# Optimization experiments

Measured on AMD Instinct MI355X. Metric: run time of the kernel, lower is better.

## Reference

```python
import jax, jax.numpy as jnp
import numpy as np

P = 16        # patch size
SIM = 0.3     # similarity threshold (forward default arg `sim`)
STY_STD = 1000.0


def patchify(imgs):
    # (N,3,H,W) -> (N, h*w, p*p*3)
    N, C, H, W = imgs.shape
    h, w = H // P, W // P
    x = imgs.reshape(N, C, h, P, w, P)
    x = jnp.einsum('nchpwq->nhwpqc', x)
    return x.reshape(N, h * w, P * P * C)


def setup_inputs() -> dict:
    key = jax.random.key(0)
    k1, k2, k3, k4 = jax.random.split(key, 4)
    N, L, D = 2, 196, 768
    x = jax.random.normal(k1, (N, L + 1, D), dtype=jnp.float32)
    imgs = jax.random.normal(k2, (N, 3, 224, 224), dtype=jnp.float32)
    # torch trunc_normal_(std=1000, a=-2, b=2) == truncated normal on [-2,2]
    learnable_sty = (jax.random.truncated_normal(
        k3, -2.0 / STY_STD, 2.0 / STY_STD, (N, L, L, 1), dtype=jnp.float32) * STY_STD)
    noise = jax.random.normal(k4, (N, L, L, 1), dtype=jnp.float32)
    return {"x": x, "imgs": imgs, "learnable_sty": learnable_sty, "noise": noise}


def reference(x, imgs, learnable_sty, noise):
    imgs = patchify(imgs)                                   # (N, L, 768)
    cls_tokens, x = x[:, :1], x[:, 1:]
    N, L, D = x.shape

    # per-patch normalization (torch.var default is unbiased -> ddof=1)
    mean = imgs.mean(axis=-1, keepdims=True)
    var = jnp.var(imgs, axis=-1, keepdims=True, ddof=1)
    imgs_n = (imgs - mean) / jnp.sqrt(var + 1e-6)
    nrm = jnp.linalg.norm(imgs_n, axis=-1)                  # (N, L)
    Sim = jnp.einsum('aik,ajk->aij', imgs_n, imgs_n) / (nrm[:, :, None] * nrm[:, None, :])

    M0 = jnp.triu((Sim > SIM).astype(jnp.float32))          # (N, L, L), binary
    rows = jnp.arange(L)

    def body(i, M):
        # original loop breaks when sum == N*L; we freeze M once that holds
        done = M.sum() == N * L
        mask = (M[:, i, :] == 0).astype(M.dtype)            # (N, L)
        # rows <= i unchanged (M*M == M for binary), rows > i masked
        upd = jnp.where(rows[None, :, None] > i, M * mask[:, None, :], M)
        return jnp.where(done, M, upd)

    M = jax.lax.fori_loop(0, L - 1, body, M0)

    # decompose: phase (con) keeps grad, amplitude (sty) is detached
    fft = jnp.fft.fftn(x, axes=(-1,))
    con, sty = jnp.angle(fft), jnp.abs(fft)
    sty_d = jax.lax.stop_gradient(sty)

    avg_sum = (M[..., None] * sty_d[:, None, :, :]).sum(axis=2)   # (N, L, D)
    sty_mask = (avg_sum > 0).astype(jnp.float32)                   # (N, L, D)
    num = M.sum(axis=2)[..., None]                                 # (N, L, 1)
    avg = avg_sum / jnp.clip(num, 1e-7, None)                      # (N, L, D)
    std = jnp.sqrt(
        (M[..., None] * (sty_d[:, None, :, :] - avg[:, :, None, :]) ** 2).sum(axis=2)
        / jnp.clip(num, 1e-7, None))                               # (N, L, D)

    sty_para = sty_mask[:, None, :, :] * learnable_sty             # (N, L, L, D)
    sty_para = sty_para / jnp.clip(sty_para.sum(axis=2, keepdims=True), 1e-7, None)
    various = noise * std[:, None, :, :] + avg[:, None, :, :]      # (N, L, L, D)
    sum_sty = (sty_para * various).sum(axis=2)                     # (N, L, D)

    # compose: ifft(amp * e^{i phase}), torch .float() keeps the real part
    out = jnp.real(jnp.fft.ifftn(sum_sty * jnp.exp(1j * con), axes=(-1,))).astype(jnp.float32)
    return jnp.concatenate((cls_tokens, out), axis=1)
```

## Files before the change

### kernel.cpp

```cpp
#include <hip/hip_runtime.h>
#include <math.h>

typedef unsigned long long u64;

#define NBATCH 2
#define LTOK 196
#define DDIM 768
#define NLD (NBATCH*LTOK*DDIM)

#ifndef M_PI
#define M_PI 3.14159265358979323846
#endif

#define S3 0.86602540378443864676f

__global__ __launch_bounds__(256) void k_patch(const float* __restrict__ imgs,
                                               float* __restrict__ u) {
  int blk = blockIdx.x;
  int a = blk / LTOK, l = blk - a * LTOK;
  int hh = l / 14, ww = l - hh * 14;
  int t = threadIdx.x;
  float loc[3];
  double s = 0.0, sq = 0.0;
#pragma unroll
  for (int e = 0; e < 3; e++) {
    int d = t + (e << 8);
    int p = d / 48, r = d - p * 48;
    int q2 = r / 3, c = r - q2 * 3;
    float val = imgs[((size_t)(a * 3 + c) * 224 + (hh * 16 + p)) * 224 + (ww * 16 + q2)];
    loc[e] = val;
    s += (double)val;
    sq += (double)val * (double)val;
  }
#pragma unroll
  for (int o = 32; o > 0; o >>= 1) { s += __shfl_down(s, o); sq += __shfl_down(sq, o); }
  __shared__ double rs[4], rq[4];
  __shared__ float sh_mu, sh_sc;
  if ((t & 63) == 0) { rs[t >> 6] = s; rq[t >> 6] = sq; }
  __syncthreads();
  if (t == 0) {
    double S = rs[0] + rs[1] + rs[2] + rs[3];
    double Q = rq[0] + rq[1] + rq[2] + rq[3];
    double mean = S / 768.0;
    double ss = Q - S * S / 768.0;
    if (ss < 1e-30) ss = 1e-30;
    sh_mu = (float)mean;
    sh_sc = (float)(1.0 / sqrt(ss));
  }
  __syncthreads();
  float mu = sh_mu, sc = sh_sc;
  size_t base = ((size_t)a * LTOK + l) * DDIM;
#pragma unroll
  for (int e = 0; e < 3; e++) { int d = t + (e << 8); u[base + d] = (loc[e] - mu) * sc; }
}

__device__ __forceinline__ void fft_butterfly(float* re, float* im,
                                              const float2* T,
                                              int tau, int s, int m, int half) {
  int sub = tau >> 7;
  int b = tau & 127;
  int j = b & (half - 1);
  int p0 = (sub << 8) + ((b >> (s - 1)) << s) + j;
  int p1 = p0 + half;
  float2 w = T[j << (8 - s)];
  float xr = re[p1], xi = im[p1];
  float tr = w.x * xr - w.y * xi;
  float ti = w.x * xi + w.y * xr;
  float ur = re[p0], ui = im[p0];
  re[p0] = ur + tr; im[p0] = ui + ti;
  re[p1] = ur - tr; im[p1] = ui - ti;
}

__device__ __forceinline__ void fft_stages(float* re, float* im,
                                           const float2* T, int t) {
#pragma unroll
  for (int s = 1; s <= 8; s++) {
    int m = 1 << s, half = m >> 1;
    fft_butterfly(re, im, T, t, s, m, half);
    if (t < 128) fft_butterfly(re, im, T, t + 256, s, m, half);
    __syncthreads();
  }
}

__global__ __launch_bounds__(256) void k_fft(const float* __restrict__ x,
                                             float* __restrict__ sty,
                                             float* __restrict__ phre,
                                             float* __restrict__ phim) {
  int blk = blockIdx.x;
  int a = blk / LTOK, i = blk - a * LTOK;
  __shared__ float re[768], im[768];
  __shared__ float2 tw768[512];
  __shared__ float2 t256[128];
  int t = threadIdx.x;
  for (int q = t; q < 512; q += 256) {
    double ang = -2.0 * M_PI * (double)q / 768.0;
    tw768[q] = make_float2((float)cos(ang), (float)sin(ang));
  }
  if (t < 128) {
    double ang = -2.0 * M_PI * (double)t / 256.0;
    t256[t] = make_float2((float)cos(ang), (float)sin(ang));
  }
  size_t row = ((size_t)a * (LTOK + 1) + 1 + i) * DDIM;
#pragma unroll
  for (int e = 0; e < 3; e++) {
    int d = t + (e << 8);
    int m = d / 3, r = d - 3 * m;
    int p = (r << 8) + (__brev((unsigned)m) >> 24);
    re[p] = x[row + d];
    im[p] = 0.f;
  }
  __syncthreads();
  fft_stages(re, im, t256, t);
  float a0r = re[t],       a0i = im[t];
  float a1r = re[256 + t], a1i = im[256 + t];
  float a2r = re[512 + t], a2i = im[512 + t];
  float2 w1 = tw768[t], w2 = tw768[2 * t];
  float b1r = a1r * w1.x - a1i * w1.y, b1i = a1r * w1.y + a1i * w1.x;
  float b2r = a2r * w2.x - a2i * w2.y, b2i = a2r * w2.y + a2i * w2.x;
  float Xr[3], Xi[3];
  Xr[0] = a0r + b1r + b2r;
  Xi[0] = a0i + b1i + b2i;
  Xr[1] = a0r + (-0.5f * b1r + S3 * b1i) + (-0.5f * b2r - S3 * b2i);
  Xi[1] = a0i + (-0.5f * b1i - S3 * b1r) + (-0.5f * b2i + S3 * b2r);
  Xr[2] = a0r + (-0.5f * b1r - S3 * b1i) + (-0.5f * b2r + S3 * b2i);
  Xi[2] = a0i + (-0.5f * b1i + S3 * b1r) + (-0.5f * b2i - S3 * b2r);
  size_t ob = ((size_t)a * LTOK + i) * DDIM + t;
#pragma unroll
  for (int s = 0; s < 3; s++) {
    float mag = sqrtf(Xr[s] * Xr[s] + Xi[s] * Xi[s]);
    size_t o = ob + (s << 8);
    sty[o] = mag;
    if (mag > 0.f) { phre[o] = Xr[s] / mag; phim[o] = Xi[s] / mag; }
    else           { phre[o] = 1.f;         phim[o] = 0.f;         }
  }
}

__global__ __launch_bounds__(256) void k_ifft(const float* __restrict__ x,
                                              const float* __restrict__ ssum,
                                              const float* __restrict__ phre,
                                              const float* __restrict__ phim,
                                              float* __restrict__ out) {
  int blk = blockIdx.x;
  int t = threadIdx.x;
  if (blk < NBATCH) {
    size_t b = (size_t)blk * (LTOK + 1) * DDIM;
    out[b + t] = x[b + t];
    out[b + t + 256] = x[b + t + 256];
    out[b + t + 512] = x[b + t + 512];
    return;
  }
  int rr = blk - NBATCH;
  int a = rr / LTOK, i = rr - a * LTOK;
  __shared__ float re[768], im[768];
  __shared__ float2 tw768[512];
  __shared__ float2 t256[128];
  for (int q = t; q < 512; q += 256) {
    double ang = 2.0 * M_PI * (double)q / 768.0;
    tw768[q] = make_float2((float)cos(ang), (float)sin(ang));
  }
  if (t < 128) {
    double ang = 2.0 * M_PI * (double)t / 256.0;
    t256[t] = make_float2((float)cos(ang), (float)sin(ang));
  }
  size_t rowz = ((size_t)a * LTOK + i) * DDIM;
#pragma unroll
  for (int e = 0; e < 3; e++) {
    int d = t + (e << 8);
    int m = d / 3, r = d - 3 * m;
    int p = (r << 8) + (__brev((unsigned)m) >> 24);
    float mg = ssum[rowz + d];
    re[p] = mg * phre[rowz + d];
    im[p] = mg * phim[rowz + d];
  }
  __syncthreads();
  fft_stages(re, im, t256, t);
  float a0r = re[t],       a0i = im[t];
  float a1r = re[256 + t], a1i = im[256 + t];
  float a2r = re[512 + t], a2i = im[512 + t];
  float2 w1 = tw768[t], w2 = tw768[2 * t];
  float b1r = a1r * w1.x - a1i * w1.y, b1i = a1r * w1.y + a1i * w1.x;
  float b2r = a2r * w2.x - a2i * w2.y, b2i = a2r * w2.y + a2i * w2.x;
  float Xr[3];
  Xr[0] = a0r + b1r + b2r;
  Xr[1] = a0r + (-0.5f * b1r - S3 * b1i) + (-0.5f * b2r + S3 * b2i);
  Xr[2] = a0r + (-0.5f * b1r + S3 * b1i) + (-0.5f * b2r - S3 * b2i);
  size_t ob = ((size_t)a * (LTOK + 1) + 1 + i) * DDIM + t;
  const float inv = 1.0f / 768.0f;
  out[ob]       = Xr[0] * inv;
  out[ob + 256] = Xr[1] * inv;
  out[ob + 512] = Xr[2] * inv;
}

__global__ __launch_bounds__(256) void k_sim(const float* __restrict__ u,
                                             u64* __restrict__ Mb) {
  int blk = blockIdx.x;
  int a = blk / LTOK, i = blk - a * LTOK;
  __shared__ float ui[768];
  __shared__ u64 mask[4];
  int t = threadIdx.x;
  if (t < 4) mask[t] = 0ull;
#pragma unroll
  for (int e = 0; e < 3; e++) { int d = t + (e << 8); ui[d] = u[((size_t)a * LTOK + i) * DDIM + d]; }
  __syncthreads();
  int j = i + t;
  if (j < LTOK) {
    const float4* uj4 = (const float4*)(u + ((size_t)a * LTOK + j) * DDIM);
    const float4* ui4 = (const float4*)ui;
    float dot = 0.f;
    for (int q = 0; q < 192; q++) {
      float4 vj = uj4[q];
      float4 vi = ui4[q];
      dot += vi.x * vj.x + vi.y * vj.y + vi.z * vj.z + vi.w * vj.w;
    }
    if (dot > 0.3f) atomicOr(&mask[j >> 6], 1ull << (j & 63));
  }
  __syncthreads();
  if (t < 4) Mb[((size_t)a * LTOK + i) * 4 + t] = mask[t];
}

__global__ __launch_bounds__(256) void k_greedy(u64* __restrict__ Mb) {
  __shared__ u64 Ml[NBATCH * LTOK * 4];
  __shared__ int red[4];
  __shared__ int Sdone;
  int t = threadIdx.x;
  for (int w = t; w < NBATCH * LTOK * 4; w += 256) Ml[w] = Mb[w];
  __syncthreads();
  for (int i = 0; i < LTOK - 1; i++) {
    int s = 0;
    for (int w = t; w < NBATCH * LTOK * 4; w += 256) s += __popcll(Ml[w]);
#pragma unroll
    for (int o = 32; o > 0; o >>= 1) s += __shfl_down(s, o);
    if ((t & 63) == 0) red[t >> 6] = s;
    __syncthreads();
    if (t == 0) Sdone = ((red[0] + red[1] + red[2] + red[3]) == NBATCH * LTOK) ? 1 : 0;
    __syncthreads();
    if (Sdone) break;
    for (int w = t; w < NBATCH * LTOK * 4; w += 256) {
      int a = w / (LTOK * 4);
      int rem = w - a * (LTOK * 4);
      int r = rem >> 2, wi = rem & 3;
      if (r > i) Ml[w] &= ~Ml[(a * LTOK + i) * 4 + wi];
    }
    __syncthreads();
  }
  for (int w = t; w < NBATCH * LTOK * 4; w += 256) Mb[w] = Ml[w];
}

__global__ __launch_bounds__(256) void k_stats(const u64* __restrict__ Mb,
                                               const float* __restrict__ sty,
                                               float* __restrict__ savg,
                                               float* __restrict__ sstd,
                                               float* __restrict__ smsk) {
  int blk = blockIdx.x;
  int a = blk / LTOK, i = blk - a * LTOK;
  __shared__ u64 mrow[4];
  int t = threadIdx.x;
  if (t < 4) mrow[t] = Mb[((size_t)a * LTOK + i) * 4 + t];
  __syncthreads();
  int num = __popcll(mrow[0]) + __popcll(mrow[1]) + __popcll(mrow[2]) + __popcll(mrow[3]);
  float fnum = fmaxf((float)num, 1e-7f);
  float acc0 = 0.f, acc1 = 0.f, acc2 = 0.f;
  for (int w = 0; w < 4; w++) {
    u64 m = mrow[w];
    while (m) {
      int b = __ffsll(m) - 1; m &= (m - 1);
      int j = (w << 6) + b;
      const float* sr = sty + ((size_t)a * LTOK + j) * DDIM;
      acc0 += sr[t]; acc1 += sr[t + 256]; acc2 += sr[t + 512];
    }
  }
  float av0 = acc0 / fnum, av1 = acc1 / fnum, av2 = acc2 / fnum;
  float sq0 = 0.f, sq1 = 0.f, sq2 = 0.f;
  for (int w = 0; w < 4; w++) {
    u64 m = mrow[w];
    while (m) {
      int b = __ffsll(m) - 1; m &= (m - 1);
      int j = (w << 6) + b;
      const float* sr = sty + ((size_t)a * LTOK + j) * DDIM;
      float d0 = sr[t] - av0, d1 = sr[t + 256] - av1, d2 = sr[t + 512] - av2;
      sq0 += d0 * d0; sq1 += d1 * d1; sq2 += d2 * d2;
    }
  }
  size_t o = ((size_t)a * LTOK + i) * DDIM + t;
  float mk0 = acc0 > 0.f ? 1.f : 0.f;
  float mk1 = acc1 > 0.f ? 1.f : 0.f;
  float mk2 = acc2 > 0.f ? 1.f : 0.f;
  smsk[o] = mk0;            smsk[o + 256] = mk1;            smsk[o + 512] = mk2;
  savg[o] = mk0 * av0;      savg[o + 256] = mk1 * av1;      savg[o + 512] = mk2 * av2;
  sstd[o] = mk0 * sqrtf(sq0 / fnum);
  sstd[o + 256] = mk1 * sqrtf(sq1 / fnum);
  sstd[o + 512] = mk2 * sqrtf(sq2 / fnum);
}

__global__ __launch_bounds__(256) void k_combine(const float* __restrict__ ls,
                                                 const float* __restrict__ nz,
                                                 const float* __restrict__ savg,
                                                 const float* __restrict__ sstd,
                                                 const float* __restrict__ smsk,
                                                 float* __restrict__ ssum) {
  int blk = blockIdx.x;
  int a = blk / 147;
  int rem = blk - a * 147;
  int it = rem / 3, dc = rem - it * 3;
  int i0 = it * 4;
  int t = threadIdx.x;
  int d = (dc << 8) + t;
  __shared__ float lsr[4][LTOK], lnr[4][LTOK];
  for (int idx = t; idx < 4 * LTOK; idx += 256) {
    int ii = idx / LTOK, j = idx - ii * LTOK;
    size_t o = ((size_t)(a * LTOK + i0 + ii)) * LTOK + j;
    float l = ls[o];
    lsr[ii][j] = l;
    lnr[ii][j] = l * nz[o];
  }
  __syncthreads();
  float a1[4] = {0.f, 0.f, 0.f, 0.f};
  float a2[4] = {0.f, 0.f, 0.f, 0.f};
  float dn[4] = {0.f, 0.f, 0.f, 0.f};
  for (int j = 0; j < LTOK; j++) {
    size_t b = ((size_t)a * LTOK + j) * DDIM + d;
    float sd = sstd[b], sv = savg[b], sm = smsk[b];
#pragma unroll
    for (int ii = 0; ii < 4; ii++) {
      a1[ii] += lnr[ii][j] * sd;
      a2[ii] += lsr[ii][j] * sv;
      dn[ii] += lsr[ii][j] * sm;
    }
  }
#pragma unroll
  for (int ii = 0; ii < 4; ii++) {
    size_t o = ((size_t)(a * LTOK + i0 + ii)) * DDIM + d;
    ssum[o] = (a1[ii] + a2[ii]) / fmaxf(dn[ii], 1e-7f);
  }
}

extern "C" void kernel_launch(void* const* d_in, const int* in_sizes, int n_in,
                              void* d_out, int out_size, void* d_ws, size_t ws_size,
                              hipStream_t stream) {
  (void)in_sizes; (void)n_in; (void)out_size; (void)ws_size;
  const float* x    = (const float*)d_in[0];
  const float* imgs = (const float*)d_in[1];
  const float* ls   = (const float*)d_in[2];
  const float* nz   = (const float*)d_in[3];
  float* out = (float*)d_out;

  float* wf   = (float*)d_ws;
  float* u    = wf;
  float* sty  = wf + (size_t)NLD;
  float* phre = wf + 2 * (size_t)NLD;
  float* phim = wf + 3 * (size_t)NLD;
  float* sstd = wf + 4 * (size_t)NLD;
  float* smsk = wf + 5 * (size_t)NLD;
  u64* Mb = (u64*)(wf + 6 * (size_t)NLD);

  k_patch  <<<NBATCH * LTOK, 256, 0, stream>>>(imgs, u);
  k_fft    <<<NBATCH * LTOK, 256, 0, stream>>>(x, sty, phre, phim);
  k_sim    <<<NBATCH * LTOK, 256, 0, stream>>>(u, Mb);
  k_greedy <<<1, 256, 0, stream>>>(Mb);
  k_stats  <<<NBATCH * LTOK, 256, 0, stream>>>(Mb, sty, u , sstd, smsk);
  k_combine<<<NBATCH * 49 * 3, 256, 0, stream>>>(ls, nz, u , sstd, smsk, sty );
  k_ifft   <<<NBATCH + NBATCH * LTOK, 256, 0, stream>>>(x, sty , phre, phim, out);
}
```

Measured before the change: 149.5 us.

## Fuse patch-norm and FFT kernels, transpose patch layout, retile combine

Merges the patch normalization and forward FFT into one launch with split block roles. The normalized patches are stored transposed so that adjacent threads in the similarity kernel read adjacent addresses. Twiddle tables computed in double precision are replaced by fast __sincosf calls, and the combine kernel now handles 7 rows per block instead of 4. Together these aim to cut launch count, uncoalesced loads and twiddle setup cost, at the price of slightly less accurate twiddles and more registers in combine.

```diff
diff --git a/kernel.cpp b/kernel.cpp
--- a/kernel.cpp
+++ b/kernel.cpp
@@ -6,57 +6,19 @@
 #define NBATCH 2
 #define LTOK 196
 #define DDIM 768
+#define NROWS (NBATCH*LTOK)
 #define NLD (NBATCH*LTOK*DDIM)
 
 #ifndef M_PI
 #define M_PI 3.14159265358979323846
 #endif
+#define PI_F 3.14159265358979323846f
 
 #define S3 0.86602540378443864676f
-
-__global__ __launch_bounds__(256) void k_patch(const float* __restrict__ imgs,
-                                               float* __restrict__ u) {
-  int blk = blockIdx.x;
-  int a = blk / LTOK, l = blk - a * LTOK;
-  int hh = l / 14, ww = l - hh * 14;
-  int t = threadIdx.x;
-  float loc[3];
-  double s = 0.0, sq = 0.0;
-#pragma unroll
-  for (int e = 0; e < 3; e++) {
-    int d = t + (e << 8);
-    int p = d / 48, r = d - p * 48;
-    int q2 = r / 3, c = r - q2 * 3;
-    float val = imgs[((size_t)(a * 3 + c) * 224 + (hh * 16 + p)) * 224 + (ww * 16 + q2)];
-    loc[e] = val;
-    s += (double)val;
-    sq += (double)val * (double)val;
-  }
-#pragma unroll
-  for (int o = 32; o > 0; o >>= 1) { s += __shfl_down(s, o); sq += __shfl_down(sq, o); }
-  __shared__ double rs[4], rq[4];
-  __shared__ float sh_mu, sh_sc;
-  if ((t & 63) == 0) { rs[t >> 6] = s; rq[t >> 6] = sq; }
-  __syncthreads();
-  if (t == 0) {
-    double S = rs[0] + rs[1] + rs[2] + rs[3];
-    double Q = rq[0] + rq[1] + rq[2] + rq[3];
-    double mean = S / 768.0;
-    double ss = Q - S * S / 768.0;
-    if (ss < 1e-30) ss = 1e-30;
-    sh_mu = (float)mean;
-    sh_sc = (float)(1.0 / sqrt(ss));
-  }
-  __syncthreads();
-  float mu = sh_mu, sc = sh_sc;
-  size_t base = ((size_t)a * LTOK + l) * DDIM;
-#pragma unroll
-  for (int e = 0; e < 3; e++) { int d = t + (e << 8); u[base + d] = (loc[e] - mu) * sc; }
-}
 
 __device__ __forceinline__ void fft_butterfly(float* re, float* im,
                                               const float2* T,
-                                              int tau, int s, int m, int half) {
+                                              int tau, int s, int half) {
   int sub = tau >> 7;
   int b = tau & 127;
   int j = b & (half - 1);
@@ -75,63 +37,250 @@
                                            const float2* T, int t) {
 #pragma unroll
   for (int s = 1; s <= 8; s++) {
-    int m = 1 << s, half = m >> 1;
-    fft_butterfly(re, im, T, t, s, m, half);
-    if (t < 128) fft_butterfly(re, im, T, t + 256, s, m, half);
-    __syncthreads();
-  }
-}
-
-__global__ __launch_bounds__(256) void k_fft(const float* __restrict__ x,
+    int half = 1 << (s - 1);
+    fft_butterfly(re, im, T, t, s, half);
+    if (t < 128) fft_butterfly(re, im, T, t + 256, s, half);
+    __syncthreads();
+  }
+}
+
+__global__ __launch_bounds__(256) void k_pre(const float* __restrict__ imgs,
+                                             const float* __restrict__ x,
+                                             float* __restrict__ uT,
                                              float* __restrict__ sty,
                                              float* __restrict__ phre,
                                              float* __restrict__ phim) {
+  int t = threadIdx.x;
+  if (blockIdx.x < NROWS) {
+    int blk = blockIdx.x;
+    int a = blk / LTOK, l = blk - a * LTOK;
+    int hh = l / 14, ww = l - hh * 14;
+    float loc[3];
+    double s = 0.0, sq = 0.0;
+#pragma unroll
+    for (int e = 0; e < 3; e++) {
+      int d = t + (e << 8);
+      int p = d / 48, r = d - p * 48;
+      int q2 = r / 3, c = r - q2 * 3;
+      float val = imgs[((size_t)(a * 3 + c) * 224 + (hh * 16 + p)) * 224 + (ww * 16 + q2)];
+      loc[e] = val;
+      s += (double)val;
+      sq += (double)val * (double)val;
+    }
+#pragma unroll
+    for (int o = 32; o > 0; o >>= 1) { s += __shfl_down(s, o); sq += __shfl_down(sq, o); }
+    __shared__ double rs[4], rq[4];
+    __shared__ float sh_mu, sh_sc;
+    if ((t & 63) == 0) { rs[t >> 6] = s; rq[t >> 6] = sq; }
+    __syncthreads();
+    if (t == 0) {
+      double S = rs[0] + rs[1] + rs[2] + rs[3];
+      double Q = rq[0] + rq[1] + rq[2] + rq[3];
+      double mean = S / 768.0;
+      double ss = Q - S * S / 768.0;
+      if (ss < 1e-30) ss = 1e-30;
+      sh_mu = (float)mean;
+      sh_sc = (float)(1.0 / sqrt(ss));
+    }
+    __syncthreads();
+    float mu = sh_mu, sc = sh_sc;
+    int col = a * LTOK + l;
+#pragma unroll
+    for (int e = 0; e < 3; e++) {
+      int d = t + (e << 8);
+      uT[(size_t)d * NROWS + col] = (loc[e] - mu) * sc;
+    }
+  } else {
+    int blk = blockIdx.x - NROWS;
+    int a = blk / LTOK, i = blk - a * LTOK;
+    __shared__ float re[768], im[768];
+    __shared__ float2 t256[128];
+    if (t < 128) {
+      float sn, cs;
+      __sincosf(-2.0f * PI_F * (float)t / 256.0f, &sn, &cs);
+      t256[t] = make_float2(cs, sn);
+    }
+    size_t row = ((size_t)a * (LTOK + 1) + 1 + i) * DDIM;
+#pragma unroll
+    for (int e = 0; e < 3; e++) {
+      int d = t + (e << 8);
+      int m = d / 3, r = d - 3 * m;
+      int p = (r << 8) + (__brev((unsigned)m) >> 24);
+      re[p] = x[row + d];
+      im[p] = 0.f;
+    }
+    __syncthreads();
+    fft_stages(re, im, t256, t);
+    float a0r = re[t],       a0i = im[t];
+    float a1r = re[256 + t], a1i = im[256 + t];
+    float a2r = re[512 + t], a2i = im[512 + t];
+    float sn, cs;
+    __sincosf(-2.0f * PI_F * (float)t / 768.0f, &sn, &cs);
+    float2 w1 = make_float2(cs, sn);
+    float2 w2 = make_float2(cs * cs - sn * sn, 2.f * cs * sn);
+    float b1r = a1r * w1.x - a1i * w1.y, b1i = a1r * w1.y + a1i * w1.x;
+    float b2r = a2r * w2.x - a2i * w2.y, b2i = a2r * w2.y + a2i * w2.x;
+    float Xr[3], Xi[3];
+    Xr[0] = a0r + b1r + b2r;
+    Xi[0] = a0i + b1i + b2i;
+    Xr[1] = a0r + (-0.5f * b1r + S3 * b1i) + (-0.5f * b2r - S3 * b2i);
+    Xi[1] = a0i + (-0.5f * b1i - S3 * b1r) + (-0.5f * b2i + S3 * b2r);
+    Xr[2] = a0r + (-0.5f * b1r - S3 * b1i) + (-0.5f * b2r + S3 * b2i);
+    Xi[2] = a0i + (-0.5f * b1i + S3 * b1r) + (-0.5f * b2i - S3 * b2r);
+    size_t ob = ((size_t)a * LTOK + i) * DDIM + t;
+#pragma unroll
+    for (int s = 0; s < 3; s++) {
+      float mag = sqrtf(Xr[s] * Xr[s] + Xi[s] * Xi[s]);
+      size_t o = ob + (s << 8);
+      sty[o] = mag;
+      if (mag > 0.f) { phre[o] = Xr[s] / mag; phim[o] = Xi[s] / mag; }
+      else           { phre[o] = 1.f;         phim[o] = 0.f;         }
+    }
+  }
+}
+
+__global__ __launch_bounds__(256) void k_sim(const float* __restrict__ uT,
+                                             u64* __restrict__ Mb) {
   int blk = blockIdx.x;
   int a = blk / LTOK, i = blk - a * LTOK;
-  __shared__ float re[768], im[768];
-  __shared__ float2 tw768[512];
-  __shared__ float2 t256[128];
-  int t = threadIdx.x;
-  for (int q = t; q < 512; q += 256) {
-    double ang = -2.0 * M_PI * (double)q / 768.0;
-    tw768[q] = make_float2((float)cos(ang), (float)sin(ang));
-  }
-  if (t < 128) {
-    double ang = -2.0 * M_PI * (double)t / 256.0;
-    t256[t] = make_float2((float)cos(ang), (float)sin(ang));
-  }
-  size_t row = ((size_t)a * (LTOK + 1) + 1 + i) * DDIM;
+  __shared__ float ui[768];
+  __shared__ u64 mask[4];
+  int t = threadIdx.x;
+  if (t < 4) mask[t] = 0ull;
+  int coli = a * LTOK + i;
 #pragma unroll
   for (int e = 0; e < 3; e++) {
     int d = t + (e << 8);
-    int m = d / 3, r = d - 3 * m;
-    int p = (r << 8) + (__brev((unsigned)m) >> 24);
-    re[p] = x[row + d];
-    im[p] = 0.f;
-  }
-  __syncthreads();
-  fft_stages(re, im, t256, t);
-  float a0r = re[t],       a0i = im[t];
-  float a1r = re[256 + t], a1i = im[256 + t];
-  float a2r = re[512 + t], a2i = im[512 + t];
-  float2 w1 = tw768[t], w2 = tw768[2 * t];
-  float b1r = a1r * w1.x - a1i * w1.y, b1i = a1r * w1.y + a1i * w1.x;
-  float b2r = a2r * w2.x - a2i * w2.y, b2i = a2r * w2.y + a2i * w2.x;
-  float Xr[3], Xi[3];
-  Xr[0] = a0r + b1r + b2r;
-  Xi[0] = a0i + b1i + b2i;
-  Xr[1] = a0r + (-0.5f * b1r + S3 * b1i) + (-0.5f * b2r - S3 * b2i);
-  Xi[1] = a0i + (-0.5f * b1i - S3 * b1r) + (-0.5f * b2i + S3 * b2r);
-  Xr[2] = a0r + (-0.5f * b1r - S3 * b1i) + (-0.5f * b2r + S3 * b2i);
-  Xi[2] = a0i + (-0.5f * b1i + S3 * b1r) + (-0.5f * b2i - S3 * b2r);
-  size_t ob = ((size_t)a * LTOK + i) * DDIM + t;
-#pragma unroll
-  for (int s = 0; s < 3; s++) {
-    float mag = sqrtf(Xr[s] * Xr[s] + Xi[s] * Xi[s]);
-    size_t o = ob + (s << 8);
-    sty[o] = mag;
-    if (mag > 0.f) { phre[o] = Xr[s] / mag; phim[o] = Xi[s] / mag; }
-    else           { phre[o] = 1.f;         phim[o] = 0.f;         }
+    ui[d] = uT[(size_t)d * NROWS + coli];
+  }
+  __syncthreads();
+  int j = i + t;
+  if (j < LTOK) {
+    const float* col = uT + (a * LTOK + j);
+    float dot = 0.f;
+#pragma unroll 8
+    for (int d = 0; d < 768; d++) dot += ui[d] * col[(size_t)d * NROWS];
+    if (dot > 0.3f) atomicOr(&mask[j >> 6], 1ull << (j & 63));
+  }
+  __syncthreads();
+  if (t < 4) Mb[((size_t)a * LTOK + i) * 4 + t] = mask[t];
+}
+
+__global__ __launch_bounds__(256) void k_greedy(u64* __restrict__ Mb) {
+  __shared__ u64 Ml[NROWS * 4];
+  __shared__ int red[4];
+  __shared__ int Sdone;
+  int t = threadIdx.x;
+  for (int w = t; w < NROWS * 4; w += 256) Ml[w] = Mb[w];
+  __syncthreads();
+  for (int i = 0; i < LTOK - 1; i++) {
+    int s = 0;
+    for (int w = t; w < NROWS * 4; w += 256) s += __popcll(Ml[w]);
+#pragma unroll
+    for (int o = 32; o > 0; o >>= 1) s += __shfl_down(s, o);
+    if ((t & 63) == 0) red[t >> 6] = s;
+    __syncthreads();
+    if (t == 0) Sdone = ((red[0] + red[1] + red[2] + red[3]) == NROWS) ? 1 : 0;
+    __syncthreads();
+    if (Sdone) break;
+    for (int w = t; w < NROWS * 4; w += 256) {
+      int a = w / (LTOK * 4);
+      int rem = w - a * (LTOK * 4);
+      int r = rem >> 2, wi = rem & 3;
+      if (r > i) Ml[w] &= ~Ml[(a * LTOK + i) * 4 + wi];
+    }
+    __syncthreads();
+  }
+  for (int w = t; w < NROWS * 4; w += 256) Mb[w] = Ml[w];
+}
+
+__global__ __launch_bounds__(256) void k_stats(const u64* __restrict__ Mb,
+                                               const float* __restrict__ sty,
+                                               float* __restrict__ savg,
+                                               float* __restrict__ sstd,
+                                               float* __restrict__ smsk) {
+  int blk = blockIdx.x;
+  int a = blk / LTOK, i = blk - a * LTOK;
+  __shared__ u64 mrow[4];
+  int t = threadIdx.x;
+  if (t < 4) mrow[t] = Mb[((size_t)a * LTOK + i) * 4 + t];
+  __syncthreads();
+  int num = __popcll(mrow[0]) + __popcll(mrow[1]) + __popcll(mrow[2]) + __popcll(mrow[3]);
+  float fnum = fmaxf((float)num, 1e-7f);
+  float acc0 = 0.f, acc1 = 0.f, acc2 = 0.f;
+  for (int w = 0; w < 4; w++) {
+    u64 m = mrow[w];
+    while (m) {
+      int b = __ffsll(m) - 1; m &= (m - 1);
+      int j = (w << 6) + b;
+      const float* sr = sty + ((size_t)a * LTOK + j) * DDIM;
+      acc0 += sr[t]; acc1 += sr[t + 256]; acc2 += sr[t + 512];
+    }
+  }
+  float av0 = acc0 / fnum, av1 = acc1 / fnum, av2 = acc2 / fnum;
+  float sq0 = 0.f, sq1 = 0.f, sq2 = 0.f;
+  for (int w = 0; w < 4; w++) {
+    u64 m = mrow[w];
+    while (m) {
+      int b = __ffsll(m) - 1; m &= (m - 1);
+      int j = (w << 6) + b;
+      const float* sr = sty + ((size_t)a * LTOK + j) * DDIM;
+      float d0 = sr[t] - av0, d1 = sr[t + 256] - av1, d2 = sr[t + 512] - av2;
+      sq0 += d0 * d0; sq1 += d1 * d1; sq2 += d2 * d2;
+    }
+  }
+  size_t o = ((size_t)a * LTOK + i) * DDIM + t;
+  float mk0 = acc0 > 0.f ? 1.f : 0.f;
+  float mk1 = acc1 > 0.f ? 1.f : 0.f;
+  float mk2 = acc2 > 0.f ? 1.f : 0.f;
+  smsk[o] = mk0;            smsk[o + 256] = mk1;            smsk[o + 512] = mk2;
+  savg[o] = mk0 * av0;      savg[o + 256] = mk1 * av1;      savg[o + 512] = mk2 * av2;
+  sstd[o] = mk0 * sqrtf(sq0 / fnum);
+  sstd[o + 256] = mk1 * sqrtf(sq1 / fnum);
+  sstd[o + 512] = mk2 * sqrtf(sq2 / fnum);
+}
+
+#define RTILE 7
+__global__ __launch_bounds__(256) void k_combine(const float* __restrict__ ls,
+                                                 const float* __restrict__ nz,
+                                                 const float* __restrict__ savg,
+                                                 const float* __restrict__ sstd,
+                                                 const float* __restrict__ smsk,
+                                                 float* __restrict__ ssum) {
+  int blk = blockIdx.x;
+  int a = blk / 84;
+  int rem = blk - a * 84;
+  int it = rem / 3, dc = rem - it * 3;
+  int i0 = it * RTILE;
+  int t = threadIdx.x;
+  int d = (dc << 8) + t;
+  __shared__ float lsr[RTILE][LTOK], lnr[RTILE][LTOK];
+  for (int idx = t; idx < RTILE * LTOK; idx += 256) {
+    int ii = idx / LTOK, j = idx - ii * LTOK;
+    size_t o = ((size_t)(a * LTOK + i0 + ii)) * LTOK + j;
+    float l = ls[o];
+    lsr[ii][j] = l;
+    lnr[ii][j] = l * nz[o];
+  }
+  __syncthreads();
+  float a1[RTILE], a2[RTILE], dn[RTILE];
+#pragma unroll
+  for (int ii = 0; ii < RTILE; ii++) { a1[ii] = 0.f; a2[ii] = 0.f; dn[ii] = 0.f; }
+#pragma unroll 2
+  for (int j = 0; j < LTOK; j++) {
+    size_t b = ((size_t)a * LTOK + j) * DDIM + d;
+    float sd = sstd[b], sv = savg[b], sm = smsk[b];
+#pragma unroll
+    for (int ii = 0; ii < RTILE; ii++) {
+      a1[ii] += lnr[ii][j] * sd;
+      a2[ii] += lsr[ii][j] * sv;
+      dn[ii] += lsr[ii][j] * sm;
+    }
+  }
+#pragma unroll
+  for (int ii = 0; ii < RTILE; ii++) {
+    size_t o = ((size_t)(a * LTOK + i0 + ii)) * DDIM + d;
+    ssum[o] = (a1[ii] + a2[ii]) / fmaxf(dn[ii], 1e-7f);
   }
 }
 
@@ -152,15 +301,11 @@
   int rr = blk - NBATCH;
   int a = rr / LTOK, i = rr - a * LTOK;
   __shared__ float re[768], im[768];
-  __shared__ float2 tw768[512];
   __shared__ float2 t256[128];
-  for (int q = t; q < 512; q += 256) {
-    double ang = 2.0 * M_PI * (double)q / 768.0;
-    tw768[q] = make_float2((float)cos(ang), (float)sin(ang));
-  }
   if (t < 128) {
-    double ang = 2.0 * M_PI * (double)t / 256.0;
-    t256[t] = make_float2((float)cos(ang), (float)sin(ang));
+    float sn, cs;
+    __sincosf(2.0f * PI_F * (float)t / 256.0f, &sn, &cs);
+    t256[t] = make_float2(cs, sn);
   }
   size_t rowz = ((size_t)a * LTOK + i) * DDIM;
 #pragma unroll
@@ -177,7 +322,10 @@
   float a0r = re[t],       a0i = im[t];
   float a1r = re[256 + t], a1i = im[256 + t];
   float a2r = re[512 + t], a2i = im[512 + t];
-  float2 w1 = tw768[t], w2 = tw768[2 * t];
+  float sn, cs;
+  __sincosf(2.0f * PI_F * (float)t / 768.0f, &sn, &cs);
+  float2 w1 = make_float2(cs, sn);
+  float2 w2 = make_float2(cs * cs - sn * sn, 2.f * cs * sn);
   float b1r = a1r * w1.x - a1i * w1.y, b1i = a1r * w1.y + a1i * w1.x;
   float b2r = a2r * w2.x - a2i * w2.y, b2i = a2r * w2.y + a2i * w2.x;
   float Xr[3];
@@ -191,149 +339,6 @@
   out[ob + 512] = Xr[2] * inv;
 }
 
-__global__ __launch_bounds__(256) void k_sim(const float* __restrict__ u,
-                                             u64* __restrict__ Mb) {
-  int blk = blockIdx.x;
-  int a = blk / LTOK, i = blk - a * LTOK;
-  __shared__ float ui[768];
-  __shared__ u64 mask[4];
-  int t = threadIdx.x;
-  if (t < 4) mask[t] = 0ull;
-#pragma unroll
-  for (int e = 0; e < 3; e++) { int d = t + (e << 8); ui[d] = u[((size_t)a * LTOK + i) * DDIM + d]; }
-  __syncthreads();
-  int j = i + t;
-  if (j < LTOK) {
-    const float4* uj4 = (const float4*)(u + ((size_t)a * LTOK + j) * DDIM);
-    const float4* ui4 = (const float4*)ui;
-    float dot = 0.f;
-    for (int q = 0; q < 192; q++) {
-      float4 vj = uj4[q];
-      float4 vi = ui4[q];
-      dot += vi.x * vj.x + vi.y * vj.y + vi.z * vj.z + vi.w * vj.w;
-    }
-    if (dot > 0.3f) atomicOr(&mask[j >> 6], 1ull << (j & 63));
-  }
-  __syncthreads();
-  if (t < 4) Mb[((size_t)a * LTOK + i) * 4 + t] = mask[t];
-}
-
-__global__ __launch_bounds__(256) void k_greedy(u64* __restrict__ Mb) {
-  __shared__ u64 Ml[NBATCH * LTOK * 4];
-  __shared__ int red[4];
-  __shared__ int Sdone;
-  int t = threadIdx.x;
-  for (int w = t; w < NBATCH * LTOK * 4; w += 256) Ml[w] = Mb[w];
-  __syncthreads();
-  for (int i = 0; i < LTOK - 1; i++) {
-    int s = 0;
-    for (int w = t; w < NBATCH * LTOK * 4; w += 256) s += __popcll(Ml[w]);
-#pragma unroll
-    for (int o = 32; o > 0; o >>= 1) s += __shfl_down(s, o);
-    if ((t & 63) == 0) red[t >> 6] = s;
-    __syncthreads();
-    if (t == 0) Sdone = ((red[0] + red[1] + red[2] + red[3]) == NBATCH * LTOK) ? 1 : 0;
-    __syncthreads();
-    if (Sdone) break;
-    for (int w = t; w < NBATCH * LTOK * 4; w += 256) {
-      int a = w / (LTOK * 4);
-      int rem = w - a * (LTOK * 4);
-      int r = rem >> 2, wi = rem & 3;
-      if (r > i) Ml[w] &= ~Ml[(a * LTOK + i) * 4 + wi];
-    }
-    __syncthreads();
-  }
-  for (int w = t; w < NBATCH * LTOK * 4; w += 256) Mb[w] = Ml[w];
-}
-
-__global__ __launch_bounds__(256) void k_stats(const u64* __restrict__ Mb,
-                                               const float* __restrict__ sty,
-                                               float* __restrict__ savg,
-                                               float* __restrict__ sstd,
-                                               float* __restrict__ smsk) {
-  int blk = blockIdx.x;
-  int a = blk / LTOK, i = blk - a * LTOK;
-  __shared__ u64 mrow[4];
-  int t = threadIdx.x;
-  if (t < 4) mrow[t] = Mb[((size_t)a * LTOK + i) * 4 + t];
-  __syncthreads();
-  int num = __popcll(mrow[0]) + __popcll(mrow[1]) + __popcll(mrow[2]) + __popcll(mrow[3]);
-  float fnum = fmaxf((float)num, 1e-7f);
-  float acc0 = 0.f, acc1 = 0.f, acc2 = 0.f;
-  for (int w = 0; w < 4; w++) {
-    u64 m = mrow[w];
-    while (m) {
-      int b = __ffsll(m) - 1; m &= (m - 1);
-      int j = (w << 6) + b;
-      const float* sr = sty + ((size_t)a * LTOK + j) * DDIM;
-      acc0 += sr[t]; acc1 += sr[t + 256]; acc2 += sr[t + 512];
-    }
-  }
-  float av0 = acc0 / fnum, av1 = acc1 / fnum, av2 = acc2 / fnum;
-  float sq0 = 0.f, sq1 = 0.f, sq2 = 0.f;
-  for (int w = 0; w < 4; w++) {
-    u64 m = mrow[w];
-    while (m) {
-      int b = __ffsll(m) - 1; m &= (m - 1);
-      int j = (w << 6) + b;
-      const float* sr = sty + ((size_t)a * LTOK + j) * DDIM;
-      float d0 = sr[t] - av0, d1 = sr[t + 256] - av1, d2 = sr[t + 512] - av2;
-      sq0 += d0 * d0; sq1 += d1 * d1; sq2 += d2 * d2;
-    }
-  }
-  size_t o = ((size_t)a * LTOK + i) * DDIM + t;
-  float mk0 = acc0 > 0.f ? 1.f : 0.f;
-  float mk1 = acc1 > 0.f ? 1.f : 0.f;
-  float mk2 = acc2 > 0.f ? 1.f : 0.f;
-  smsk[o] = mk0;            smsk[o + 256] = mk1;            smsk[o + 512] = mk2;
-  savg[o] = mk0 * av0;      savg[o + 256] = mk1 * av1;      savg[o + 512] = mk2 * av2;
-  sstd[o] = mk0 * sqrtf(sq0 / fnum);
-  sstd[o + 256] = mk1 * sqrtf(sq1 / fnum);
-  sstd[o + 512] = mk2 * sqrtf(sq2 / fnum);
-}
-
-__global__ __launch_bounds__(256) void k_combine(const float* __restrict__ ls,
-                                                 const float* __restrict__ nz,
-                                                 const float* __restrict__ savg,
-                                                 const float* __restrict__ sstd,
-                                                 const float* __restrict__ smsk,
-                                                 float* __restrict__ ssum) {
-  int blk = blockIdx.x;
-  int a = blk / 147;
-  int rem = blk - a * 147;
-  int it = rem / 3, dc = rem - it * 3;
-  int i0 = it * 4;
-  int t = threadIdx.x;
-  int d = (dc << 8) + t;
-  __shared__ float lsr[4][LTOK], lnr[4][LTOK];
-  for (int idx = t; idx < 4 * LTOK; idx += 256) {
-    int ii = idx / LTOK, j = idx - ii * LTOK;
-    size_t o = ((size_t)(a * LTOK + i0 + ii)) * LTOK + j;
-    float l = ls[o];
-    lsr[ii][j] = l;
-    lnr[ii][j] = l * nz[o];
-  }
-  __syncthreads();
-  float a1[4] = {0.f, 0.f, 0.f, 0.f};
-  float a2[4] = {0.f, 0.f, 0.f, 0.f};
-  float dn[4] = {0.f, 0.f, 0.f, 0.f};
-  for (int j = 0; j < LTOK; j++) {
-    size_t b = ((size_t)a * LTOK + j) * DDIM + d;
-    float sd = sstd[b], sv = savg[b], sm = smsk[b];
-#pragma unroll
-    for (int ii = 0; ii < 4; ii++) {
-      a1[ii] += lnr[ii][j] * sd;
-      a2[ii] += lsr[ii][j] * sv;
-      dn[ii] += lsr[ii][j] * sm;
-    }
-  }
-#pragma unroll
-  for (int ii = 0; ii < 4; ii++) {
-    size_t o = ((size_t)(a * LTOK + i0 + ii)) * DDIM + d;
-    ssum[o] = (a1[ii] + a2[ii]) / fmaxf(dn[ii], 1e-7f);
-  }
-}
-
 extern "C" void kernel_launch(void* const* d_in, const int* in_sizes, int n_in,
                               void* d_out, int out_size, void* d_ws, size_t ws_size,
                               hipStream_t stream) {
@@ -345,7 +350,7 @@
   float* out = (float*)d_out;
 
   float* wf   = (float*)d_ws;
-  float* u    = wf;
+  float* uT   = wf;
   float* sty  = wf + (size_t)NLD;
   float* phre = wf + 2 * (size_t)NLD;
   float* phim = wf + 3 * (size_t)NLD;
@@ -353,11 +358,10 @@
   float* smsk = wf + 5 * (size_t)NLD;
   u64* Mb = (u64*)(wf + 6 * (size_t)NLD);
 
-  k_patch  <<<NBATCH * LTOK, 256, 0, stream>>>(imgs, u);
-  k_fft    <<<NBATCH * LTOK, 256, 0, stream>>>(x, sty, phre, phim);
-  k_sim    <<<NBATCH * LTOK, 256, 0, stream>>>(u, Mb);
+  k_pre    <<<2 * NROWS, 256, 0, stream>>>(imgs, x, uT, sty, phre, phim);
+  k_sim    <<<NROWS, 256, 0, stream>>>(uT, Mb);
   k_greedy <<<1, 256, 0, stream>>>(Mb);
-  k_stats  <<<NBATCH * LTOK, 256, 0, stream>>>(Mb, sty, u , sstd, smsk);
-  k_combine<<<NBATCH * 49 * 3, 256, 0, stream>>>(ls, nz, u , sstd, smsk, sty );
-  k_ifft   <<<NBATCH + NBATCH * LTOK, 256, 0, stream>>>(x, sty , phre, phim, out);
-}
+  k_stats  <<<NROWS, 256, 0, stream>>>(Mb, sty, uT , sstd, smsk);
+  k_combine<<<NBATCH * 28 * 3, 256, 0, stream>>>(ls, nz, uT , sstd, smsk, sty );
+  k_ifft   <<<NBATCH + NROWS, 256, 0, stream>>>(x, sty , phre, phim, out);
+}
```

Measured after the change: 145.5 us. -2.7%, faster.
